# Kernel optimization log

Measured on AMD Instinct MI355X. Metric: run time of the kernel, lower is better.

Reference implementation:

```python
import jax, jax.numpy as jnp
import numpy as np

SEQ, B, V, E, H, L, S_SRC = 128, 32, 32000, 1024, 1024, 3, 64


def setup_inputs() -> dict:
    key = jax.random.key(0)
    ks = jax.random.split(key, 8)
    sc = 0.05
    return {
        "tokens": jax.random.randint(ks[0], (SEQ, B), 0, V),
        "emb_W": jax.random.normal(ks[1], (V, E), jnp.float32) * 0.1,
        "W_ih": jax.random.normal(ks[2], (L, 4 * H, E), jnp.float32) * sc,
        "W_hh": jax.random.normal(ks[3], (L, 4 * H, H), jnp.float32) * sc,
        "b_ih": jnp.zeros((L, 4 * H), jnp.float32),
        "b_hh": jnp.zeros((L, 4 * H), jnp.float32),
        "attn_Win": jax.random.normal(ks[4], (E, E), jnp.float32) * sc,
        "attn_Wout": jax.random.normal(ks[5], (E, 2 * E), jnp.float32) * sc,
        "final_b": jnp.zeros((V,), jnp.float32),
        "encoder_outs": jax.random.normal(ks[6], (S_SRC, B, E), jnp.float32),
        "h0": jnp.zeros((L, B, H), jnp.float32),
        "c0": jnp.zeros((L, B, H), jnp.float32),
    }


def reference(tokens, emb_W, W_ih, W_hh, b_ih, b_hh, attn_Win, attn_Wout,
              final_b, encoder_outs, h0, c0):
    # Eval mode: all dropouts (dropoute/i/h/out) are identity.
    emb = emb_W[tokens]                                  # [SEQ, B, E]
    ctx = jnp.transpose(encoder_outs, (1, 0, 2))         # [B, S_src, E]

    def lstm_cell(x, h, c, l):
        gates = x @ W_ih[l].T + b_ih[l] + h @ W_hh[l].T + b_hh[l]  # [B, 4H]
        i, f, g, o = jnp.split(gates, 4, axis=-1)        # torch order: i,f,g,o
        i, f, o = jax.nn.sigmoid(i), jax.nn.sigmoid(f), jax.nn.sigmoid(o)
        g = jnp.tanh(g)
        c_new = f * c + i * g
        return o * jnp.tanh(c_new), c_new

    def step(carry, x_t):
        h, c = carry                                     # each [L, B, H]
        hs, cs = [], []
        inp = x_t
        for l in range(L):
            h_new, c_new = lstm_cell(inp, h[l], c[l], l)
            hs.append(h_new)
            cs.append(c_new)
            inp = h_new                                  # dropouth is identity
        # SoftDotAttention on last layer hidden
        target = h_new @ attn_Win.T                      # [B, E]
        attn = jax.nn.softmax(jnp.einsum('bse,be->bs', ctx, target), axis=-1)
        wc = jnp.einsum('bs,bse->be', attn, ctx)         # weighted context
        h_tilde = jnp.tanh(jnp.concatenate([wc, h_new], axis=-1) @ attn_Wout.T)
        return (jnp.stack(hs), jnp.stack(cs)), h_tilde

    (_, _), outs = jax.lax.scan(step, (h0, c0), emb)     # outs: [SEQ, B, E]
    logits = outs @ emb_W.T + final_b                    # tied weights: [SEQ, B, V]
    return logits
```

## Files before the change

kernel.cpp:

```cpp
#include <hip/hip_runtime.h>
#include <cstdint>
#include <cstddef>

#define SEQ   128
#define BB    32
#define EE    1024
#define HH    1024
#define G4    4096
#define VV    32000
#define NROWS 4096

typedef _Float16 h16x8 __attribute__((ext_vector_type(8)));
typedef _Float16 h16x4 __attribute__((ext_vector_type(4)));
typedef float f32x4  __attribute__((ext_vector_type(4)));

#define AS_G(p) ((const __attribute__((address_space(1))) void*)(p))
#define AS_L(p) ((__attribute__((address_space(3))) void*)(p))

__device__ __forceinline__ float sigmf(float x) { return 1.0f / (1.0f + expf(-x)); }

#define OFF_SYNC    0ull
#define OFF_HFRAG0  40960ull
#define OFF_EMB     630784ull
#define OFF_WIH0    9019392ull
#define OFF_TARGET  17408000ull
#define OFF_HT      25796608ull
#define OFF_HFRAGH  630784ull
#define OFF_X0      34185216ull
#define OFF_WP4     67739648ull
#define OFF_WP0     101294080ull
#define OFF_EMBW    109682688ull
#define OFF_WIN     175218688ull
#define OFF_WOUT    177315840ull
#define OFF_ENC     181510144ull
#define OFF_H2ALL   185704448ull
#define OFF_CONCAT  194093056ull
#define WS_NEEDED   210870272ull

__global__ __launch_bounds__(256) void k_conv(const float* __restrict__ s,
                                              _Float16* __restrict__ d, int n4) {
  int i = blockIdx.x * blockDim.x + threadIdx.x;
  int st = gridDim.x * blockDim.x;
  for (; i < n4; i += st) {
    float4 v = ((const float4*)s)[i];
    h16x4 o; o[0] = (_Float16)v.x; o[1] = (_Float16)v.y; o[2] = (_Float16)v.z; o[3] = (_Float16)v.w;
    ((h16x4*)d)[i] = o;
  }
}

__global__ __launch_bounds__(256) void k_gather(const int* __restrict__ tok,
                                                const float* __restrict__ embW,
                                                _Float16* __restrict__ emb) {
  int row = blockIdx.x;
  int t = tok[row];
  float4 v = ((const float4*)(embW + (size_t)t * EE))[threadIdx.x];
  h16x4 o; o[0] = (_Float16)v.x; o[1] = (_Float16)v.y; o[2] = (_Float16)v.z; o[3] = (_Float16)v.w;
  ((h16x4*)(emb + (size_t)row * EE))[threadIdx.x] = o;
}

__global__ __launch_bounds__(256) void k_packw4(const float* __restrict__ Wih,
                                                const float* __restrict__ Whh,
                                                _Float16* __restrict__ out) {
  int i = blockIdx.x * blockDim.x + threadIdx.x;
  int st = gridDim.x * blockDim.x;
  const int total = 256 * 65536;
  for (; i < total; i += st) {
    int w = i >> 16, rem = i & 65535;
    int wp = (w & 7) * 32 + (w >> 3);
    int mat = rem >> 14, jj = (rem >> 10) & 15, k = rem & 1023;
    int layer = 1 + (mat >> 1), isHH = mat & 1;
    int row = ((jj >> 2) << 10) + (wp << 2) + (jj & 3);
    int ks = k ^ ((jj & 7) << 3);
    const float* src = (isHH ? Whh : Wih) + (size_t)layer * G4 * 1024 + (size_t)row * 1024 + ks;
    out[i] = (_Float16)(*src);
  }
}

__global__ __launch_bounds__(256) void k_packw0(const float* __restrict__ Whh,
                                                _Float16* __restrict__ out) {
  int i = blockIdx.x * blockDim.x + threadIdx.x;
  int st = gridDim.x * blockDim.x;
  const int total = 256 * 16384;
  for (; i < total; i += st) {
    int w = i >> 14, rem = i & 16383;
    int wp = (w & 7) * 32 + (w >> 3);
    int ks = rem >> 9, lane = (rem >> 3) & 63, e = rem & 7;
    int jj = lane & 15, q = lane >> 4;
    int row = ((jj >> 2) << 10) + (wp << 2) + (jj & 3);
    int k = ks * 32 + q * 8 + e;
    out[i] = (_Float16)Whh[(size_t)row * 1024 + k];
  }
}

__global__ __launch_bounds__(256) void k_init(const float* __restrict__ h0,
                                              _Float16* __restrict__ hfrag0,
                                              unsigned* __restrict__ sync) {
  int i = blockIdx.x * blockDim.x + threadIdx.x;
  if (i < 64 + 8192) sync[i] = 0u;
  if (i >= 3 * BB * HH) return;
  int l = i >> 15, rem = i & 32767;
  int b = rem >> 10, n = rem & 1023;
  int tbb = b >> 4, ks = n >> 5, q = (n >> 3) & 3, e = n & 7;
  int lane2 = (b & 15) | (q << 4);
  hfrag0[(size_t)l * 131072 + ((size_t)(tbb * 32 + ks) * 64 + lane2) * 8 + e] =
      (_Float16)h0[i];
}

template <int EPI>
__global__ __launch_bounds__(256) void k_gemm(const _Float16* __restrict__ A,
                                              const _Float16* __restrict__ B,
                                              void* __restrict__ C, int M, int N, int K,
                                              const float* __restrict__ bias1,
                                              const float* __restrict__ bias2) {
  __shared__ _Float16 As[2][128 * 32];
  __shared__ _Float16 Bs[2][128 * 32];
  const int ntn = N / 128;
  const int nwg = gridDim.x;
  const int bid = (blockIdx.x & 7) * (nwg >> 3) + (blockIdx.x >> 3);
  const int tm = bid / ntn, tn = bid % ntn;
  const int tid = threadIdx.x, lane = tid & 63;
  const int wv = tid >> 6, wr = wv >> 1, wc = wv & 1;
  f32x4 acc[4][4] = {};

  auto stage = [&](int buf, int k0) {
#pragma unroll
    for (int i = 0; i < 2; ++i) {
      int eo = (i * 256 + tid) * 8;
      int r = eo >> 5, c = eo & 31;
      __builtin_amdgcn_global_load_lds(AS_G(A + (size_t)(tm * 128 + r) * K + k0 + c),
                                       AS_L(&As[buf][eo]), 16, 0, 0);
      __builtin_amdgcn_global_load_lds(AS_G(B + (size_t)(tn * 128 + r) * K + k0 + c),
                                       AS_L(&Bs[buf][eo]), 16, 0, 0);
    }
  };
  stage(0, 0);
  __syncthreads();
  const int nk = K / 32;
  for (int kt = 0; kt < nk; ++kt) {
    if (kt + 1 < nk) stage((kt + 1) & 1, (kt + 1) * 32);
    const int buf = kt & 1;
    h16x8 af[4], bfr[4];
#pragma unroll
    for (int mi = 0; mi < 4; ++mi)
      af[mi] = *(const h16x8*)&As[buf][(wr * 64 + mi * 16 + (lane & 15)) * 32 + (lane >> 4) * 8];
#pragma unroll
    for (int ni = 0; ni < 4; ++ni)
      bfr[ni] = *(const h16x8*)&Bs[buf][(wc * 64 + ni * 16 + (lane & 15)) * 32 + (lane >> 4) * 8];
#pragma unroll
    for (int mi = 0; mi < 4; ++mi)
#pragma unroll
      for (int ni = 0; ni < 4; ++ni)
        acc[mi][ni] = __builtin_amdgcn_mfma_f32_16x16x32_f16(af[mi], bfr[ni], acc[mi][ni], 0, 0, 0);
    __syncthreads();
  }
  const int rbase = tm * 128 + wr * 64;
  const int cbase = tn * 128 + wc * 64;
#pragma unroll
  for (int mi = 0; mi < 4; ++mi) {
#pragma unroll
    for (int ni = 0; ni < 4; ++ni) {
#pragma unroll
      for (int r = 0; r < 4; ++r) {
        int mm = rbase + mi * 16 + (lane >> 4) * 4 + r;
        int nn = cbase + ni * 16 + (lane & 15);
        float v = acc[mi][ni][r];
        if (EPI == 1) {
          ((_Float16*)C)[(size_t)mm * N + nn] = (_Float16)v;
        } else {
          ((_Float16*)C)[(size_t)mm * N + nn] = (_Float16)tanhf(v);
        }
      }
    }
  }
}

template <int EPI>
__global__ __launch_bounds__(512, 2) void k_gemm256(const _Float16* __restrict__ A,
                                                    const _Float16* __restrict__ B,
                                                    void* __restrict__ C, int M, int N, int K,
                                                    const float* __restrict__ bias1,
                                                    const float* __restrict__ bias2) {
  extern __shared__ char glds[];
  _Float16* Asl = (_Float16*)glds;
  _Float16* Bsl = (_Float16*)(glds + 3 * 8192 * 2);
  const int ntn = N / 256;
  const int nwg = gridDim.x;
  const int bid = (blockIdx.x & 7) * (nwg >> 3) + (blockIdx.x >> 3);
  const int tm = bid / ntn, tn = bid % ntn;
  const int tid = threadIdx.x, lane = tid & 63;
  const int wid = tid >> 6, wm = wid >> 2, wn = wid & 3;
  const int fr = lane & 15, fc = lane >> 4;
  const int srow0 = tid >> 2, sg = tid & 3;

  f32x4 acc[8][4] = {};
  const int nt = K / 32;

  auto stage = [&](int t) {
    const int slot = t % 3;
    const size_t kof = (size_t)t * 32 + sg * 8;
#pragma unroll
    for (int r = 0; r < 2; ++r) {
      int row = r * 128 + srow0;
      __builtin_amdgcn_global_load_lds(AS_G(A + (size_t)(tm * 256 + row) * K + kof),
                                       AS_L(&Asl[slot * 8192 + row * 32 + sg * 8]), 16, 0, 0);
    }
#pragma unroll
    for (int r = 0; r < 2; ++r) {
      int row = r * 128 + srow0;
      __builtin_amdgcn_global_load_lds(AS_G(B + (size_t)(tn * 256 + row) * K + kof),
                                       AS_L(&Bsl[slot * 8192 + row * 32 + sg * 8]), 16, 0, 0);
    }
  };

  stage(0);
  stage(1);
  asm volatile("s_waitcnt vmcnt(4)" ::: "memory");
  asm volatile("s_barrier" ::: "memory");

  for (int t = 0; t < nt; ++t) {
    if (t + 2 < nt) {
      stage(t + 2);
      asm volatile("s_waitcnt vmcnt(4)" ::: "memory");
    } else {
      asm volatile("s_waitcnt vmcnt(0)" ::: "memory");
    }
    asm volatile("s_barrier" ::: "memory");
    const int slot = t % 3;
    const _Float16* as = &Asl[slot * 8192];
    const _Float16* bs = &Bsl[slot * 8192];
    h16x8 af[8], bf[4];
#pragma unroll
    for (int mi = 0; mi < 8; ++mi)
      af[mi] = *(const h16x8*)&as[(wm * 128 + mi * 16 + fr) * 32 + fc * 8];
#pragma unroll
    for (int ni = 0; ni < 4; ++ni)
      bf[ni] = *(const h16x8*)&bs[(wn * 64 + ni * 16 + fr) * 32 + fc * 8];
    __builtin_amdgcn_s_setprio(1);
#pragma unroll
    for (int mi = 0; mi < 8; ++mi)
#pragma unroll
      for (int ni = 0; ni < 4; ++ni)
        acc[mi][ni] = __builtin_amdgcn_mfma_f32_16x16x32_f16(af[mi], bf[ni], acc[mi][ni], 0, 0, 0);
    __builtin_amdgcn_s_setprio(0);
    asm volatile("s_barrier" ::: "memory");
  }

  const int rbase = tm * 256 + wm * 128;
  const int cbase = tn * 256 + wn * 64;
#pragma unroll
  for (int mi = 0; mi < 8; ++mi) {
#pragma unroll
    for (int ni = 0; ni < 4; ++ni) {
#pragma unroll
      for (int r = 0; r < 4; ++r) {
        int mm = rbase + mi * 16 + fc * 4 + r;
        int nn = cbase + ni * 16 + fr;
        float v = acc[mi][ni][r];
        if (EPI == 0) {
          ((float*)C)[(size_t)mm * N + nn] = v + bias1[nn];
        } else {
          ((_Float16*)C)[(size_t)mm * N + nn] = (_Float16)(v + bias1[nn] + bias2[nn]);
        }
      }
    }
  }
}

__global__ __launch_bounds__(512) void k_recur(const _Float16* __restrict__ Wp4,
                                               const _Float16* __restrict__ Wp0,
                                               const _Float16* __restrict__ X0bf,
                                               _Float16* __restrict__ hfrag0,
                                               _Float16* __restrict__ hfragH,
                                               _Float16* __restrict__ h2all,
                                               _Float16* __restrict__ concat,
                                               const float* __restrict__ bih,
                                               const float* __restrict__ bhh,
                                               const float* __restrict__ c0p,
                                               unsigned* __restrict__ sync) {
  extern __shared__ char lds[];
  _Float16* ldsW = (_Float16*)lds;
  float* redbuf = (float*)(lds + 131072);
  _Float16* hstage = (_Float16*)(lds + 131072);
  float* gbuf = (float*)(lds + 149504);
  unsigned* arrive = sync + 64;

  const int w = blockIdx.x;
  const int wp = (w & 7) * 32 + (w >> 3);
  const int tid = threadIdx.x, lane = tid & 63, wv = tid >> 6;
  const int tb = wv & 1, kq = wv >> 1;
  const int row = (lane >> 4) * 4, col = lane & 15;

  for (int i = 0; i < 16; ++i) {
    int eo = (i * 512 + tid) * 8;
    *(h16x8*)&ldsW[eo] = *(const h16x8*)(Wp4 + (size_t)w * 65536 + eo);
  }
  h16x8 w0reg[8];
#pragma unroll
  for (int i = 0; i < 8; ++i)
    w0reg[i] = *(const h16x8*)(Wp0 + (size_t)w * 16384 + ((size_t)(kq * 8 + i) * 64 + lane) * 8);

  const int eb = tid >> 2, eni = tid & 3, en = wp * 4 + eni;
  float c0r = 0.f, c1r = 0.f, c2r = 0.f;
  float b1r[4] = {0, 0, 0, 0}, b2r[4] = {0, 0, 0, 0};
  if (tid < 128) {
    c0r = c0p[0 * BB * HH + eb * HH + en];
    c1r = c0p[1 * BB * HH + eb * HH + en];
    c2r = c0p[2 * BB * HH + eb * HH + en];
#pragma unroll
    for (int g = 0; g < 4; ++g) {
      b1r[g] = bih[1 * G4 + g * 1024 + en] + bhh[1 * G4 + g * 1024 + en];
      b2r[g] = bih[2 * G4 + g * 1024 + en] + bhh[2 * G4 + g * 1024 + en];
    }
  }
  const int pk_l = tid >> 5, pk_r = tid & 31;
  const size_t pk_idx = ((size_t)(((pk_r >> 4) * 32 + (wp >> 3)) * 64 + (pk_r & 15) +
                                  (((wp >> 1) & 3) << 4))) * 8 + 4 * (wp & 1);
  __syncthreads();

  for (int tau = 0; tau < 130; ++tau) {
    const _Float16* rb = (tau < 3) ? (hfrag0 + (size_t)tau * 98304)
                                   : (hfragH + (size_t)(tau - 3) * 98304);
    _Float16* wb = (tau + 1 < 3) ? (hfrag0 + (size_t)(tau + 1) * 98304)
                                 : (hfragH + (size_t)(tau - 2) * 98304);
    const _Float16* h0r = rb;
    const _Float16* h1r = rb + 32768;
    const _Float16* h2r = rb + 65536;

    h16x8 a0[8], a1[8], a2[8];
#pragma unroll
    for (int i = 0; i < 8; ++i) {
      int ks = kq * 8 + i;
      size_t off = ((size_t)(tb * 32 + ks) * 64 + lane) * 8;
      a0[i] = *(const h16x8*)(h0r + off);
      a1[i] = *(const h16x8*)(h1r + off);
      a2[i] = *(const h16x8*)(h2r + off);
    }
    float xg0 = 0.f, xg1 = 0.f, xg2 = 0.f, xg3 = 0.f;
    if (tid < 128 && tau < 128) {
      size_t xb = ((size_t)(tau * BB + eb)) * G4 + en;
      xg0 = (float)X0bf[xb];        xg1 = (float)X0bf[xb + 1024];
      xg2 = (float)X0bf[xb + 2048]; xg3 = (float)X0bf[xb + 3072];
    }
    f32x4 acc0 = {}, acc1 = {}, acc2 = {};
#pragma unroll
    for (int i = 0; i < 8; ++i) {
      int ks = kq * 8 + i;
      int jj = lane & 15, q = lane >> 4;
      int kk = (ks * 32 + q * 8) ^ ((jj & 7) << 3);
      const h16x8 bw1i = *(const h16x8*)&ldsW[0 * 16384 + jj * 1024 + kk];
      const h16x8 bw1h = *(const h16x8*)&ldsW[1 * 16384 + jj * 1024 + kk];
      const h16x8 bw2i = *(const h16x8*)&ldsW[2 * 16384 + jj * 1024 + kk];
      const h16x8 bw2h = *(const h16x8*)&ldsW[3 * 16384 + jj * 1024 + kk];
      acc0 = __builtin_amdgcn_mfma_f32_16x16x32_f16(a0[i], w0reg[i], acc0, 0, 0, 0);
      acc1 = __builtin_amdgcn_mfma_f32_16x16x32_f16(a0[i], bw1i, acc1, 0, 0, 0);
      acc1 = __builtin_amdgcn_mfma_f32_16x16x32_f16(a1[i], bw1h, acc1, 0, 0, 0);
      acc2 = __builtin_amdgcn_mfma_f32_16x16x32_f16(a1[i], bw2i, acc2, 0, 0, 0);
      acc2 = __builtin_amdgcn_mfma_f32_16x16x32_f16(a2[i], bw2h, acc2, 0, 0, 0);
    }
    if (kq >= 1) {
      int s = kq - 1;
#pragma unroll
      for (int r = 0; r < 4; ++r) {
        redbuf[((0 * 3 + s) * 2 + tb) * 256 + (row + r) * 16 + col] = acc0[r];
        redbuf[((1 * 3 + s) * 2 + tb) * 256 + (row + r) * 16 + col] = acc1[r];
        redbuf[((2 * 3 + s) * 2 + tb) * 256 + (row + r) * 16 + col] = acc2[r];
      }
    }
    __syncthreads();
    if (kq == 0) {
#pragma unroll
      for (int r = 0; r < 4; ++r) {
        float v0 = acc0[r], v1 = acc1[r], v2 = acc2[r];
#pragma unroll
        for (int s = 0; s < 3; ++s) {
          v0 += redbuf[((0 * 3 + s) * 2 + tb) * 256 + (row + r) * 16 + col];
          v1 += redbuf[((1 * 3 + s) * 2 + tb) * 256 + (row + r) * 16 + col];
          v2 += redbuf[((2 * 3 + s) * 2 + tb) * 256 + (row + r) * 16 + col];
        }
        gbuf[(0 * 32 + tb * 16 + row + r) * 16 + col] = v0;
        gbuf[(1 * 32 + tb * 16 + row + r) * 16 + col] = v1;
        gbuf[(2 * 32 + tb * 16 + row + r) * 16 + col] = v2;
      }
    }
    __syncthreads();
    if (tid < 128) {
      if (tau < 128) {
        float gi = gbuf[(0 * 32 + eb) * 16 + eni] + xg0;
        float gf = gbuf[(0 * 32 + eb) * 16 + 4 + eni] + xg1;
        float gg = gbuf[(0 * 32 + eb) * 16 + 8 + eni] + xg2;
        float go = gbuf[(0 * 32 + eb) * 16 + 12 + eni] + xg3;
        c0r = sigmf(gf) * c0r + sigmf(gi) * tanhf(gg);
        hstage[0 * 128 + tid] = (_Float16)(sigmf(go) * tanhf(c0r));
      }
      if (tau >= 1 && tau < 129) {
        float gi = gbuf[(1 * 32 + eb) * 16 + eni] + b1r[0];
        float gf = gbuf[(1 * 32 + eb) * 16 + 4 + eni] + b1r[1];
        float gg = gbuf[(1 * 32 + eb) * 16 + 8 + eni] + b1r[2];
        float go = gbuf[(1 * 32 + eb) * 16 + 12 + eni] + b1r[3];
        c1r = sigmf(gf) * c1r + sigmf(gi) * tanhf(gg);
        hstage[1 * 128 + tid] = (_Float16)(sigmf(go) * tanhf(c1r));
      }
      if (tau >= 2) {
        float gi = gbuf[(2 * 32 + eb) * 16 + eni] + b2r[0];
        float gf = gbuf[(2 * 32 + eb) * 16 + 4 + eni] + b2r[1];
        float gg = gbuf[(2 * 32 + eb) * 16 + 8 + eni] + b2r[2];
        float go = gbuf[(2 * 32 + eb) * 16 + 12 + eni] + b2r[3];
        c2r = sigmf(gf) * c2r + sigmf(gi) * tanhf(gg);
        float h = sigmf(go) * tanhf(c2r);
        _Float16 hb = (_Float16)h;
        hstage[2 * 128 + tid] = hb;
        int t2 = tau - 2;
        h2all[(size_t)(t2 * BB + eb) * HH + en] = hb;
        concat[(size_t)(t2 * BB + eb) * 2048 + 1024 + en] = hb;
      }
    }
    __syncthreads();
    {
      bool act = (tid < 96) &&
                 ((pk_l == 0) ? (tau < 128)
                  : (pk_l == 1) ? (tau >= 1 && tau < 129)
                                : (tau >= 2 && tau < 129));
      if (act) {
        unsigned long long v = *(const unsigned long long*)&hstage[pk_l * 128 + pk_r * 4];
        __hip_atomic_store(
            (unsigned long long*)(wb + (size_t)pk_l * 32768 + pk_idx), v,
            __ATOMIC_RELAXED, __HIP_MEMORY_SCOPE_AGENT);
      }
      asm volatile("s_waitcnt vmcnt(0)" ::: "memory");
    }
    __syncthreads();
    if (tid == 0)
      __hip_atomic_store(&arrive[w * 32], (unsigned)(tau + 1), __ATOMIC_RELAXED,
                         __HIP_MEMORY_SCOPE_AGENT);
    if (tau < 129) {
      if (tid < 64) {
        for (;;) {
          bool ok = true;
#pragma unroll
          for (int j = 0; j < 4; ++j) {
            unsigned v = __hip_atomic_load(&arrive[(tid * 4 + j) * 32], __ATOMIC_RELAXED,
                                           __HIP_MEMORY_SCOPE_AGENT);
            ok &= (v >= (unsigned)(tau + 1));
          }
          if (__all(ok)) break;
          __builtin_amdgcn_s_sleep(1);
        }
        asm volatile("" ::: "memory");
      }
      __syncthreads();
    }
  }
}

__global__ __launch_bounds__(256) void k_attn(const _Float16* __restrict__ target,
                                              const _Float16* __restrict__ encb,
                                              _Float16* __restrict__ concat) {
  __shared__ float sc[64];
  __shared__ float att[64];
  int m = blockIdx.x, b = m & 31;
  int tid = threadIdx.x, lane = tid & 63, wv = tid >> 6;
  const h16x8* tp = (const h16x8*)(target + (size_t)m * EE + lane * 16);
  h16x8 tg0 = tp[0], tg1 = tp[1];
  for (int si = 0; si < 16; ++si) {
    int s = wv * 16 + si;
    const h16x8* ep = (const h16x8*)(encb + ((size_t)s * BB + b) * EE + lane * 16);
    h16x8 e0 = ep[0], e1 = ep[1];
    float a = 0.f;
#pragma unroll
    for (int j = 0; j < 8; ++j) a += (float)e0[j] * (float)tg0[j];
#pragma unroll
    for (int j = 0; j < 8; ++j) a += (float)e1[j] * (float)tg1[j];
#pragma unroll
    for (int off = 32; off >= 1; off >>= 1) a += __shfl_xor(a, off);
    if (lane == 0) sc[s] = a;
  }
  __syncthreads();
  if (wv == 0) {
    float v = sc[lane], mx = v;
#pragma unroll
    for (int off = 32; off >= 1; off >>= 1) mx = fmaxf(mx, __shfl_xor(mx, off));
    float e = expf(v - mx), sm = e;
#pragma unroll
    for (int off = 32; off >= 1; off >>= 1) sm += __shfl_xor(sm, off);
    att[lane] = e / sm;
  }
  __syncthreads();
  int e4 = tid * 4;
  float a0 = 0, a1 = 0, a2 = 0, a3 = 0;
  for (int s = 0; s < 64; ++s) {
    float wgt = att[s];
    h16x4 ev = *(const h16x4*)(encb + ((size_t)s * BB + b) * EE + e4);
    a0 += wgt * (float)ev[0]; a1 += wgt * (float)ev[1];
    a2 += wgt * (float)ev[2]; a3 += wgt * (float)ev[3];
  }
  h16x4 o; o[0] = (_Float16)a0; o[1] = (_Float16)a1; o[2] = (_Float16)a2; o[3] = (_Float16)a3;
  *(h16x4*)(concat + (size_t)m * 2048 + e4) = o;
}

extern "C" void kernel_launch(void* const* d_in, const int* in_sizes, int n_in,
                              void* d_out, int out_size, void* d_ws, size_t ws_size,
                              hipStream_t stream) {
  const int* tokens = (const int*)d_in[0];
  const float* embW = (const float*)d_in[1];
  const float* Wih = (const float*)d_in[2];
  const float* Whh = (const float*)d_in[3];
  const float* bih = (const float*)d_in[4];
  const float* bhh = (const float*)d_in[5];
  const float* Win = (const float*)d_in[6];
  const float* Wout = (const float*)d_in[7];
  const float* finalb = (const float*)d_in[8];
  const float* enc = (const float*)d_in[9];
  const float* h0 = (const float*)d_in[10];
  const float* c0 = (const float*)d_in[11];
  (void)in_sizes; (void)n_in; (void)out_size;
  if (ws_size < WS_NEEDED) return;

  char* ws = (char*)d_ws;
  unsigned* sync = (unsigned*)(ws + OFF_SYNC);
  _Float16* hfrag0 = (_Float16*)(ws + OFF_HFRAG0);
  _Float16* hfragH = (_Float16*)(ws + OFF_HFRAGH);
  _Float16* emb = (_Float16*)(ws + OFF_EMB);
  _Float16* X0bf = (_Float16*)(ws + OFF_X0);
  _Float16* Wih0b = (_Float16*)(ws + OFF_WIH0);
  _Float16* Wp4 = (_Float16*)(ws + OFF_WP4);
  _Float16* Wp0 = (_Float16*)(ws + OFF_WP0);
  _Float16* embWb = (_Float16*)(ws + OFF_EMBW);
  _Float16* Winb = (_Float16*)(ws + OFF_WIN);
  _Float16* Woutb = (_Float16*)(ws + OFF_WOUT);
  _Float16* encb = (_Float16*)(ws + OFF_ENC);
  _Float16* h2all = (_Float16*)(ws + OFF_H2ALL);
  _Float16* concat = (_Float16*)(ws + OFF_CONCAT);
  _Float16* target = (_Float16*)(ws + OFF_TARGET);
  _Float16* ht = (_Float16*)(ws + OFF_HT);

  const unsigned LDSB = 155648;
  const unsigned LDSG = 98304;
  static int lds_set = 0;
  if (!lds_set) {
    hipFuncSetAttribute((const void*)k_recur, hipFuncAttributeMaxDynamicSharedMemorySize,
                        (int)LDSB);
    hipFuncSetAttribute((const void*)k_gemm256<0>, hipFuncAttributeMaxDynamicSharedMemorySize,
                        (int)LDSG);
    hipFuncSetAttribute((const void*)k_gemm256<1>, hipFuncAttributeMaxDynamicSharedMemorySize,
                        (int)LDSG);
    lds_set = 1;
  }

  k_conv<<<4096, 256, 0, stream>>>(embW, embWb, VV * EE / 4);
  k_conv<<<1024, 256, 0, stream>>>(Wih, Wih0b, G4 * EE / 4);
  k_conv<<<512, 256, 0, stream>>>(Win, Winb, EE * EE / 4);
  k_conv<<<512, 256, 0, stream>>>(Wout, Woutb, EE * 2048 / 4);
  k_conv<<<512, 256, 0, stream>>>(enc, encb, 64 * BB * EE / 4);
  k_gather<<<NROWS, 256, 0, stream>>>(tokens, embW, emb);
  k_packw4<<<8192, 256, 0, stream>>>(Wih, Whh, Wp4);
  k_packw0<<<4096, 256, 0, stream>>>(Whh, Wp0);
  k_init<<<384, 256, 0, stream>>>(h0, hfrag0, sync);

  k_gemm256<1><<<16 * 16, 512, LDSG, stream>>>(emb, Wih0b, X0bf, NROWS, G4, EE, bih, bhh);

  k_recur<<<256, 512, LDSB, stream>>>(Wp4, Wp0, X0bf, hfrag0, hfragH, h2all, concat,
                                      bih, bhh, c0, sync);

  k_gemm<1><<<32 * 8, 256, 0, stream>>>(h2all, Winb, target, NROWS, EE, EE, nullptr, nullptr);
  k_attn<<<NROWS, 256, 0, stream>>>(target, encb, concat);
  k_gemm<2><<<32 * 8, 256, 0, stream>>>(concat, Woutb, ht, NROWS, EE, 2048, nullptr, nullptr);

  k_gemm256<0><<<16 * 125, 512, LDSG, stream>>>(ht, embWb, d_out, NROWS, VV, EE, finalb, nullptr);
}
```

Baseline: 1.425 ms.

## Use 16-wave blocks in 256x256 GEMM and cache encoder tile in attention LDS

The 256x256 GEMM now runs 1024 threads per block. Each wave owns a 64x64 sub-tile instead of 128x64, and the pipeline drops from triple to double buffering with one LDS slot fewer. This roughly halves the accumulator registers per wave to raise occupancy and latency hiding, at the cost of a shallower prefetch. Separately, the attention kernel now runs one block per (batch, 16-timestep chunk). It loads that batch's 64x1024 encoder slice into 128 KB of LDS once and reuses it across 16 timesteps, instead of re-reading it from global memory for every row, at the cost of far fewer blocks.

After: 1.523 ms. 1.07x slower.

```diff
diff --git a/kernel.cpp b/kernel.cpp
--- a/kernel.cpp
+++ b/kernel.cpp
@@ -175,14 +175,14 @@
 }
 
 template <int EPI>
-__global__ __launch_bounds__(512, 2) void k_gemm256(const _Float16* __restrict__ A,
-                                                    const _Float16* __restrict__ B,
-                                                    void* __restrict__ C, int M, int N, int K,
-                                                    const float* __restrict__ bias1,
-                                                    const float* __restrict__ bias2) {
+__global__ __launch_bounds__(1024, 4) void k_gemm256(const _Float16* __restrict__ A,
+                                                     const _Float16* __restrict__ B,
+                                                     void* __restrict__ C, int M, int N, int K,
+                                                     const float* __restrict__ bias1,
+                                                     const float* __restrict__ bias2) {
   extern __shared__ char glds[];
   _Float16* Asl = (_Float16*)glds;
-  _Float16* Bsl = (_Float16*)(glds + 3 * 8192 * 2);
+  _Float16* Bsl = (_Float16*)(glds + 2 * 8192 * 2);
   const int ntn = N / 256;
   const int nwg = gridDim.x;
   const int bid = (blockIdx.x & 7) * (nwg >> 3) + (blockIdx.x >> 3);
@@ -190,54 +190,42 @@
   const int tid = threadIdx.x, lane = tid & 63;
   const int wid = tid >> 6, wm = wid >> 2, wn = wid & 3;
   const int fr = lane & 15, fc = lane >> 4;
-  const int srow0 = tid >> 2, sg = tid & 3;
-
-  f32x4 acc[8][4] = {};
+  const int srow = tid >> 2, sg = tid & 3;
+
+  f32x4 acc[4][4] = {};
   const int nt = K / 32;
 
   auto stage = [&](int t) {
-    const int slot = t % 3;
+    const int slot = t & 1;
     const size_t kof = (size_t)t * 32 + sg * 8;
-#pragma unroll
-    for (int r = 0; r < 2; ++r) {
-      int row = r * 128 + srow0;
-      __builtin_amdgcn_global_load_lds(AS_G(A + (size_t)(tm * 256 + row) * K + kof),
-                                       AS_L(&Asl[slot * 8192 + row * 32 + sg * 8]), 16, 0, 0);
-    }
-#pragma unroll
-    for (int r = 0; r < 2; ++r) {
-      int row = r * 128 + srow0;
-      __builtin_amdgcn_global_load_lds(AS_G(B + (size_t)(tn * 256 + row) * K + kof),
-                                       AS_L(&Bsl[slot * 8192 + row * 32 + sg * 8]), 16, 0, 0);
-    }
+    __builtin_amdgcn_global_load_lds(AS_G(A + (size_t)(tm * 256 + srow) * K + kof),
+                                     AS_L(&Asl[slot * 8192 + srow * 32 + sg * 8]), 16, 0, 0);
+    __builtin_amdgcn_global_load_lds(AS_G(B + (size_t)(tn * 256 + srow) * K + kof),
+                                     AS_L(&Bsl[slot * 8192 + srow * 32 + sg * 8]), 16, 0, 0);
   };
 
   stage(0);
-  stage(1);
-  asm volatile("s_waitcnt vmcnt(4)" ::: "memory");
-  asm volatile("s_barrier" ::: "memory");
-
   for (int t = 0; t < nt; ++t) {
-    if (t + 2 < nt) {
-      stage(t + 2);
-      asm volatile("s_waitcnt vmcnt(4)" ::: "memory");
+    if (t + 1 < nt) {
+      stage(t + 1);
+      asm volatile("s_waitcnt vmcnt(2)" ::: "memory");
     } else {
       asm volatile("s_waitcnt vmcnt(0)" ::: "memory");
     }
     asm volatile("s_barrier" ::: "memory");
-    const int slot = t % 3;
+    const int slot = t & 1;
     const _Float16* as = &Asl[slot * 8192];
     const _Float16* bs = &Bsl[slot * 8192];
-    h16x8 af[8], bf[4];
-#pragma unroll
-    for (int mi = 0; mi < 8; ++mi)
-      af[mi] = *(const h16x8*)&as[(wm * 128 + mi * 16 + fr) * 32 + fc * 8];
+    h16x8 af[4], bf[4];
+#pragma unroll
+    for (int mi = 0; mi < 4; ++mi)
+      af[mi] = *(const h16x8*)&as[(wm * 64 + mi * 16 + fr) * 32 + fc * 8];
 #pragma unroll
     for (int ni = 0; ni < 4; ++ni)
       bf[ni] = *(const h16x8*)&bs[(wn * 64 + ni * 16 + fr) * 32 + fc * 8];
     __builtin_amdgcn_s_setprio(1);
 #pragma unroll
-    for (int mi = 0; mi < 8; ++mi)
+    for (int mi = 0; mi < 4; ++mi)
 #pragma unroll
       for (int ni = 0; ni < 4; ++ni)
         acc[mi][ni] = __builtin_amdgcn_mfma_f32_16x16x32_f16(af[mi], bf[ni], acc[mi][ni], 0, 0, 0);
@@ -245,10 +233,10 @@
     asm volatile("s_barrier" ::: "memory");
   }
 
-  const int rbase = tm * 256 + wm * 128;
+  const int rbase = tm * 256 + wm * 64;
   const int cbase = tn * 256 + wn * 64;
 #pragma unroll
-  for (int mi = 0; mi < 8; ++mi) {
+  for (int mi = 0; mi < 4; ++mi) {
 #pragma unroll
     for (int ni = 0; ni < 4; ++ni) {
 #pragma unroll
@@ -455,46 +443,62 @@
 __global__ __launch_bounds__(256) void k_attn(const _Float16* __restrict__ target,
                                               const _Float16* __restrict__ encb,
                                               _Float16* __restrict__ concat) {
+  extern __shared__ _Float16 elds[];
   __shared__ float sc[64];
   __shared__ float att[64];
-  int m = blockIdx.x, b = m & 31;
-  int tid = threadIdx.x, lane = tid & 63, wv = tid >> 6;
-  const h16x8* tp = (const h16x8*)(target + (size_t)m * EE + lane * 16);
-  h16x8 tg0 = tp[0], tg1 = tp[1];
-  for (int si = 0; si < 16; ++si) {
-    int s = wv * 16 + si;
-    const h16x8* ep = (const h16x8*)(encb + ((size_t)s * BB + b) * EE + lane * 16);
-    h16x8 e0 = ep[0], e1 = ep[1];
-    float a = 0.f;
-#pragma unroll
-    for (int j = 0; j < 8; ++j) a += (float)e0[j] * (float)tg0[j];
-#pragma unroll
-    for (int j = 0; j < 8; ++j) a += (float)e1[j] * (float)tg1[j];
-#pragma unroll
-    for (int off = 32; off >= 1; off >>= 1) a += __shfl_xor(a, off);
-    if (lane == 0) sc[s] = a;
-  }
+  const int b = blockIdx.x >> 3, tc = blockIdx.x & 7;
+  const int tid = threadIdx.x, lane = tid & 63, wv = tid >> 6;
+
+  for (int it = 0; it < 32; ++it) {
+    int g = it * 256 + tid;
+    __builtin_amdgcn_global_load_lds(
+        AS_G(encb + ((size_t)((g >> 7) * 32 + b)) * 1024 + (g & 127) * 8),
+        AS_L(elds + (size_t)g * 8), 16, 0, 0);
+  }
+  asm volatile("s_waitcnt vmcnt(0)" ::: "memory");
   __syncthreads();
-  if (wv == 0) {
-    float v = sc[lane], mx = v;
-#pragma unroll
-    for (int off = 32; off >= 1; off >>= 1) mx = fmaxf(mx, __shfl_xor(mx, off));
-    float e = expf(v - mx), sm = e;
-#pragma unroll
-    for (int off = 32; off >= 1; off >>= 1) sm += __shfl_xor(sm, off);
-    att[lane] = e / sm;
-  }
-  __syncthreads();
-  int e4 = tid * 4;
-  float a0 = 0, a1 = 0, a2 = 0, a3 = 0;
-  for (int s = 0; s < 64; ++s) {
-    float wgt = att[s];
-    h16x4 ev = *(const h16x4*)(encb + ((size_t)s * BB + b) * EE + e4);
-    a0 += wgt * (float)ev[0]; a1 += wgt * (float)ev[1];
-    a2 += wgt * (float)ev[2]; a3 += wgt * (float)ev[3];
-  }
-  h16x4 o; o[0] = (_Float16)a0; o[1] = (_Float16)a1; o[2] = (_Float16)a2; o[3] = (_Float16)a3;
-  *(h16x4*)(concat + (size_t)m * 2048 + e4) = o;
+
+  for (int ti = 0; ti < 16; ++ti) {
+    const int m = (tc * 16 + ti) * 32 + b;
+    const h16x8* tp = (const h16x8*)(target + (size_t)m * EE + lane * 16);
+    h16x8 tg0 = tp[0], tg1 = tp[1];
+#pragma unroll 4
+    for (int si = 0; si < 16; ++si) {
+      int s = wv * 16 + si;
+      const h16x8* ep = (const h16x8*)(elds + (size_t)s * EE + lane * 16);
+      h16x8 e0 = ep[0], e1 = ep[1];
+      float a = 0.f;
+#pragma unroll
+      for (int j = 0; j < 8; ++j) a += (float)e0[j] * (float)tg0[j];
+#pragma unroll
+      for (int j = 0; j < 8; ++j) a += (float)e1[j] * (float)tg1[j];
+#pragma unroll
+      for (int off = 32; off >= 1; off >>= 1) a += __shfl_xor(a, off);
+      if (lane == 0) sc[s] = a;
+    }
+    __syncthreads();
+    if (wv == 0) {
+      float v = sc[lane], mx = v;
+#pragma unroll
+      for (int off = 32; off >= 1; off >>= 1) mx = fmaxf(mx, __shfl_xor(mx, off));
+      float e = expf(v - mx), sm = e;
+#pragma unroll
+      for (int off = 32; off >= 1; off >>= 1) sm += __shfl_xor(sm, off);
+      att[lane] = e / sm;
+    }
+    __syncthreads();
+    int e4 = tid * 4;
+    float a0 = 0, a1 = 0, a2 = 0, a3 = 0;
+    for (int s = 0; s < 64; ++s) {
+      float wgt = att[s];
+      h16x4 ev = *(const h16x4*)(elds + (size_t)s * EE + e4);
+      a0 += wgt * (float)ev[0]; a1 += wgt * (float)ev[1];
+      a2 += wgt * (float)ev[2]; a3 += wgt * (float)ev[3];
+    }
+    h16x4 o; o[0] = (_Float16)a0; o[1] = (_Float16)a1; o[2] = (_Float16)a2; o[3] = (_Float16)a3;
+    *(h16x4*)(concat + (size_t)m * 2048 + e4) = o;
+    __syncthreads();
+  }
 }
 
 extern "C" void kernel_launch(void* const* d_in, const int* in_sizes, int n_in,
@@ -534,7 +538,8 @@
   _Float16* ht = (_Float16*)(ws + OFF_HT);
 
   const unsigned LDSB = 155648;
-  const unsigned LDSG = 98304;
+  const unsigned LDSG = 65536;
+  const unsigned LDSA = 131072;
   static int lds_set = 0;
   if (!lds_set) {
     hipFuncSetAttribute((const void*)k_recur, hipFuncAttributeMaxDynamicSharedMemorySize,
@@ -543,6 +548,8 @@
                         (int)LDSG);
     hipFuncSetAttribute((const void*)k_gemm256<1>, hipFuncAttributeMaxDynamicSharedMemorySize,
                         (int)LDSG);
+    hipFuncSetAttribute((const void*)k_attn, hipFuncAttributeMaxDynamicSharedMemorySize,
+                        (int)LDSA);
     lds_set = 1;
   }
 
@@ -556,14 +563,14 @@
   k_packw0<<<4096, 256, 0, stream>>>(Whh, Wp0);
   k_init<<<384, 256, 0, stream>>>(h0, hfrag0, sync);
 
-  k_gemm256<1><<<16 * 16, 512, LDSG, stream>>>(emb, Wih0b, X0bf, NROWS, G4, EE, bih, bhh);
+  k_gemm256<1><<<16 * 16, 1024, LDSG, stream>>>(emb, Wih0b, X0bf, NROWS, G4, EE, bih, bhh);
 
   k_recur<<<256, 512, LDSB, stream>>>(Wp4, Wp0, X0bf, hfrag0, hfragH, h2all, concat,
                                       bih, bhh, c0, sync);
 
   k_gemm<1><<<32 * 8, 256, 0, stream>>>(h2all, Winb, target, NROWS, EE, EE, nullptr, nullptr);
-  k_attn<<<NROWS, 256, 0, stream>>>(target, encb, concat);
+  k_attn<<<256, 256, LDSA, stream>>>(target, encb, concat);
   k_gemm<2><<<32 * 8, 256, 0, stream>>>(concat, Woutb, ht, NROWS, EE, 2048, nullptr, nullptr);
 
-  k_gemm256<0><<<16 * 125, 512, LDSG, stream>>>(ht, embWb, d_out, NROWS, VV, EE, finalb, nullptr);
-}
+  k_gemm256<0><<<16 * 125, 1024, LDSG, stream>>>(ht, embWb, d_out, NROWS, VV, EE, finalb, nullptr);
+}
```
